# Kernel tuning notes

Hardware: AMD Instinct MI355X
Metric: run time of the kernel (lower is better)

Reference implementation:

```python
import jax, jax.numpy as jnp
import numpy as np

C_P = 1004.0
R_EARTH = 6371000.0
R_GAS = 287.0
OMEGA_E = 7.292e-05
B, K, H, W = 1, 8, 361, 720
KK = 5   # kernel basis size
D = 5    # neighborhood width in lat and lon (radius 2)
NS = K * 4 + 1
FCH = K * 4
NU = 2.0e5  # diffusion coefficient


def _ch(k, kind):
    return k * 4 + kind


def disco_gather(x, psi, quad):
    # DISCO sparse neighborhood aggregation on the sphere.
    # x: (B,C,H,W); psi: (KK,2,H,D,D) lat-dependent filter basis (2 directional comps)
    # returns (B,C,KK,2,H,W)
    Bx, C, Hx, Wx = x.shape
    Kk, nc, _, Dlat, Dlon = psi.shape
    r = Dlat // 2
    lat = np.clip(np.arange(Hx)[:, None] + np.arange(Dlat)[None, :] - r, 0, Hx - 1)
    out = jnp.zeros((Bx, C, Kk, nc, Hx, Wx), x.dtype)
    for dl in range(Dlat):
        li = lat[:, dl]
        xg = x[:, :, li, :] * quad[li][None, None, :, None]  # quadrature-weighted gather
        for dw in range(Dlon):
            xs = jnp.roll(xg, -(dw - r), axis=-1)  # circular in longitude
            out = out + psi[:, :, :, dl, dw][None, None, :, :, :, None] * xs[:, :, None, None, :, :]
    return out


def setup_inputs():
    key = jax.random.key(0)
    k1, k2, k3 = jax.random.split(key, 3)
    uv = jax.random.normal(k1, (B, K, H, W, 2), jnp.float32)
    T = jax.random.normal(k2, (B, K, H, W), jnp.float32)
    q = jax.random.normal(k3, (B, K, H, W), jnp.float32)
    rng = np.random.RandomState(0)
    psi = ((rng.rand(KK, 2, H, D, D) - 0.5) / (D * D)).astype(np.float32)
    colat = np.linspace(0.0, np.pi, H)
    quad = (np.sin(colat) * np.pi / (H - 1)).astype(np.float32)
    f_cor = (2.0 * OMEGA_E * np.sin(np.pi / 2.0 - colat)).astype(np.float32)
    p = np.array([1e5 * np.exp(-k * np.log(10.0) / (K - 1)) for k in range(K)], np.float32)
    lpr = np.log(p[:-1] / p[1:])
    p_low = np.concatenate([p[:1], 0.5 * (p[:-1] + p[1:])])
    p_up = np.concatenate([0.5 * (p[:-1] + p[1:]), [0.0]])
    dp = (p_low - p_up).astype(np.float32)
    # physics-encoded weights (module freezes all params and sets them analytically)
    W_ss_blk = np.zeros((NS, NS, KK), np.float32)
    W_vs_blk = np.zeros((NS, K, KK, 2), np.float32)
    for k in range(K):
        W_vs_blk[_ch(k, 2), k, :, 0] = 1.0 / R_EARTH  # zeta (curl)
        W_vs_blk[_ch(k, 3), k, :, 1] = 1.0 / R_EARTH  # div
    W_sv_blk = np.zeros((K, NS, KK, 2), np.float32)
    for ko in range(K):
        for ki in range(ko):
            W_sv_blk[ko, _ch(ki, 0), :, 1] = -R_GAS * lpr[ki] / R_EARTH  # PGF
        W_sv_blk[ko, _ch(ko, 1), :, 1] = -1.0 / R_EARTH  # -grad KE
    W_vv_blk = np.zeros((K, K, KK, 2), np.float32)
    W_vs2_blk = np.zeros((NS, K, KK, 2), np.float32)
    W_pw_ss = np.zeros((NS, NS), np.float32)
    W_pw_ss[FCH, FCH] = 1.0
    W_svp = np.zeros((NS, K, 2), np.float32)
    for k in range(K):
        W_svp[_ch(k, 2), k, 1] = 1.0
    W_svp[FCH, :, 1] = -1.0
    W_pw_vv = np.zeros((K, K), np.float32)
    W_ss_adv = np.zeros((2 * K, 2 * K, KK), np.float32)
    W_vs_adv = np.zeros((2 * K, K, KK, 2), np.float32)
    W_vs2_adv = np.zeros((2 * K, K, KK, 2), np.float32)
    for k in range(K):
        W_vs2_adv[k, k, :, 1] = -1.0 / R_EARTH      # -V.grad T
        W_vs2_adv[K + k, k, :, 1] = -1.0 / R_EARTH  # -V.grad q
    W_sv_grad = np.zeros((1, 1, KK, 2), np.float32)
    W_sv_grad[0, 0, :, 1] = 1.0 / R_EARTH
    W_vs_div = np.zeros((1, 1, KK, 2), np.float32)
    W_vs_div[0, 0, :, 1] = 1.0 / R_EARTH
    j = jnp.asarray
    return dict(uv=uv, T=T, q=q, psi=j(psi), quad=j(quad), f_cor=j(f_cor), p_levels=j(p), delta_p=j(dp),
                W_ss_blk=j(W_ss_blk), W_vs_blk=j(W_vs_blk), W_sv_blk=j(W_sv_blk), W_vv_blk=j(W_vv_blk),
                W_vs2_blk=j(W_vs2_blk), W_pw_ss=j(W_pw_ss), W_svp=j(W_svp), W_pw_vv=j(W_pw_vv),
                W_ss_adv=j(W_ss_adv), W_vs_adv=j(W_vs_adv), W_vs2_adv=j(W_vs2_adv),
                W_sv_grad=j(W_sv_grad), W_vs_div=j(W_vs_div))


def _forward(uv, T, q, psi, quad, f_cor, p_levels, delta_p, W_ss_blk, W_vs_blk, W_sv_blk, W_vv_blk,
             W_vs2_blk, W_pw_ss, W_svp, W_pw_vv, W_ss_adv, W_vs_adv, W_vs2_adv, W_sv_grad, W_vs_div):
    Bx, Kx, Hx, Wx = T.shape
    ke = 0.5 * (uv[..., 0] ** 2 + uv[..., 1] ** 2)
    zeros = jnp.zeros_like(T)
    per = jnp.stack([T, ke, zeros, zeros], axis=2).reshape(Bx, Kx * 4, Hx, Wx)
    f_field = jnp.broadcast_to(f_cor[None, None, :, None], (Bx, 1, Hx, Wx))
    x_s = jnp.concatenate([per, f_field], axis=1)  # (B, 4K+1, H, W)
    # ---- Block 1: VectorDiscoBlock ----
    Gs = disco_gather(x_s, psi, quad)               # (B,NS,KK,2,H,W)
    Ga = disco_gather(uv[..., 0], psi, quad)
    Gb = disco_gather(uv[..., 1], psi, quad)
    Gdir = jnp.stack([Ga[:, :, :, 0], Gb[:, :, :, 1]], axis=3)  # curl/div pairing
    Giso = jnp.stack([Ga[:, :, :, 0], Gb[:, :, :, 0]], axis=3)
    ys_c = jnp.einsum('oik,bikhw->bohw', W_ss_blk, Gs[:, :, :, 0])
    ys_c = ys_c + jnp.einsum('oikc,bikchw->bohw', W_vs_blk, Gdir)
    ys_c = ys_c + jnp.einsum('oikc,bokchw,bihwc->bohw', W_vs2_blk, Gs, uv)
    yv_c = jnp.einsum('oikc,bikchw->bohwc', W_sv_blk, Gs)
    yv_c = yv_c + jnp.einsum('oikc,bikchw->bohwc', W_vv_blk, Giso)
    s_feat = ys_c + jnp.einsum('oi,bihw->bohw', W_pw_ss, x_s)
    coef0 = jnp.einsum('ij,bihw->bjhw', W_svp[:, :, 0], s_feat)
    coef1 = jnp.einsum('ij,bihw->bjhw', W_svp[:, :, 1], s_feat)
    cross = jnp.stack([-uv[..., 1], uv[..., 0]], axis=-1)  # k-hat x V
    sv = coef0[..., None] * uv + coef1[..., None] * cross
    y_v = uv + yv_c + sv + jnp.einsum('oi,bihwc->bohwc', W_pw_vv, uv)
    y_s = s_feat
    duv_dt = y_v - uv
    # omega from divergence (upward pressure integral)
    div = y_s[:, :Kx * 4].reshape(Bx, Kx, 4, Hx, Wx)[:, :, 3]
    cum = jnp.cumsum(div * delta_p[None, :, None, None], axis=1)
    omega = 0.5 * (jnp.concatenate([jnp.zeros_like(cum[:, :1]), cum[:, :-1]], axis=1) + cum)
    # ---- adv_conv (W_vs2 pathway): -V.grad(T), -V.grad(q) ----
    tq = jnp.concatenate([T, q], axis=1)
    Gtq = disco_gather(tq, psi, quad)
    dTq = jnp.einsum('oik,bikhw->bohw', W_ss_adv, Gtq[:, :, :, 0])
    dTq = dTq + jnp.einsum('oikc,bikchw->bohw', W_vs_adv, Gdir)
    dTq = dTq + jnp.einsum('oikc,bokchw,bihwc->bohw', W_vs2_adv, Gtq, uv)
    dT_dt = dTq[:, :Kx]
    dq_dt = dTq[:, Kx:]
    # dT/dp central differences
    p = p_levels
    inter = (T[:, 2:] - T[:, :-2]) / (p[2:] - p[:-2])[None, :, None, None]
    first = (T[:, 1:2] - T[:, 0:1]) / (p[1] - p[0])
    last = (T[:, -1:] - T[:, -2:-1]) / (p[-1] - p[-2])
    dTdp = jnp.concatenate([first, inter, last], axis=1)
    pk = p[None, :, None, None]
    dT_dt = dT_dt + omega * (R_GAS / C_P * T / pk - dTdp)
    # ---- diffusion: nu * div(grad(s)) via grad_conv/div_conv ----
    def lap(s):
        sf = s.reshape(Bx * Kx, 1, Hx, Wx)
        Gsf = disco_gather(sf, psi, quad)
        g = jnp.einsum('oikc,bikchw->bohwc', W_sv_grad, Gsf)  # (BK,1,H,W,2)
        Gga = disco_gather(g[..., 0], psi, quad)
        Ggb = disco_gather(g[..., 1], psi, quad)
        Gd = jnp.stack([Gga[:, :, :, 0], Ggb[:, :, :, 1]], axis=3)
        return jnp.einsum('oikc,bikchw->bohw', W_vs_div, Gd).reshape(Bx, Kx, Hx, Wx)
    dT_dt = dT_dt + NU * lap(T)
    dq_dt = dq_dt + NU * lap(q)
    duv_dt = duv_dt + NU * jnp.stack([lap(uv[..., 0]), lap(uv[..., 1])], axis=-1)
    return duv_dt, dT_dt, dq_dt


def reference(uv, T, q, psi, quad, f_cor, p_levels, delta_p, W_ss_blk, W_vs_blk, W_sv_blk, W_vv_blk,
              W_vs2_blk, W_pw_ss, W_svp, W_pw_vv, W_ss_adv, W_vs_adv, W_vs2_adv, W_sv_grad, W_vs_div):
    return _forward(uv, T, q, psi, quad, f_cor, p_levels, delta_p, W_ss_blk, W_vs_blk, W_sv_blk,
                    W_vv_blk, W_vs2_blk, W_pw_ss, W_svp, W_pw_vv, W_ss_adv, W_vs_adv, W_vs2_adv,
                    W_sv_grad, W_vs_div)
```

## Files before the change

kernel.cpp:

```cpp
#include <hip/hip_runtime.h>


constexpr int Kz = 8, Hh = 361, Ww = 720;
constexpr int HW = Hh * Ww;
constexpr int OFF_DT = Kz * HW * 2;
constexpr int OFF_DQ = OFF_DT + Kz * HW;

constexpr int TH = 16, TW = 64;
constexpr int SH = TH + 8, SW4 = TW + 8;
constexpr int EH = TH + 4, EW4 = TW + 4;
constexpr int SW4P = 73;
constexpr int EW4P = 69;

__device__ __forceinline__ int clipH(int x) {
  return x < 0 ? 0 : (x > Hh - 1 ? Hh - 1 : x);
}

#define FMA4(acc, s, v)                                                        \
  do {                                                                         \
    acc.x = fmaf((s), (v).x, acc.x);                                           \
    acc.y = fmaf((s), (v).y, acc.y);                                           \
    acc.z = fmaf((s), (v).z, acc.z);                                           \
    acc.w = fmaf((s), (v).w, acc.w);                                           \
  } while (0)

#define ROWV(acc, a, b, c, d, e)                                               \
  do {                                                                         \
    FMA4(acc, wq0, a); FMA4(acc, wq1, b); FMA4(acc, wq2, c);                   \
    FMA4(acc, wq3, d); FMA4(acc, wq4, e);                                      \
  } while (0)

#define ROW5S(acc, q0, q1, q2, q3, q4, a, b, c, d, e)                          \
  acc = fmaf(q0, a, fmaf(q1, b, fmaf(q2, c, fmaf(q3, d, fmaf(q4, e, acc)))))

__global__ __launch_bounds__(256, 3) void pe_pass1(
    const float2* __restrict__ uv,
    const float*  __restrict__ Tg,
    const float*  __restrict__ qg,
    const float*  __restrict__ psi,
    const float*  __restrict__ quad,
    const float*  __restrict__ f_cor,
    const float*  __restrict__ delta_p,
    float* __restrict__ out,
    float2* __restrict__ ws)
{
  __shared__ float4 S4[SH][SW4P];
  __shared__ float4 d1S[EH][EW4P];
  __shared__ float P1q[EH][25];
  __shared__ float P0q[TH][25];

  const int tid = threadIdx.x;
  const int tx = tid & 15;
  const int ty = tid >> 4;
  const int w0 = blockIdx.x * TW;
  const int h0 = blockIdx.y * TH;
  const int k  = blockIdx.z;

  for (int idx = tid; idx < EH * 25; idx += 256) {
    int ee = idx / 25, t = idx - ee * 25;
    int p = clipH(h0 + ee - 2);
    int dl = t / 5;
    float s = 0.f;
    #pragma unroll
    for (int kk = 0; kk < 5; ++kk)
      s += psi[kk * (2 * Hh * 25) + Hh * 25 + p * 25 + t];
    P1q[ee][t] = s * quad[clipH(p + dl - 2)];
  }
  for (int idx = tid; idx < TH * 25; idx += 256) {
    int r = idx / 25, t = idx - r * 25;
    int p = clipH(h0 + r);
    int dl = t / 5;
    float s = 0.f;
    #pragma unroll
    for (int kk = 0; kk < 5; ++kk)
      s += psi[kk * (2 * Hh * 25) + p * 25 + t];
    P0q[r][t] = s * quad[clipH(p + dl - 2)];
  }

  for (int idx = tid; idx < SH * SW4; idx += 256) {
    int rr = idx / SW4, cc = idx - rr * SW4;
    int pr = clipH(h0 + rr - 4);
    int pc = w0 + cc - 4;
    pc = pc < 0 ? pc + Ww : (pc >= Ww ? pc - Ww : pc);
    int g = (k * Hh + pr) * Ww + pc;
    float2 uvv = uv[g];
    S4[rr][cc] = make_float4(uvv.x, uvv.y, Tg[g], qg[g]);
  }
  __syncthreads();

  for (int idx = tid; idx < EH * (EW4 / 4); idx += 256) {
    int ee = idx % EH;
    int gc = idx / EH;
    int cb = gc * 4;
    int p = clipH(h0 + ee - 2);
    float4 a0 = {0,0,0,0}, a1 = {0,0,0,0}, a2 = {0,0,0,0}, a3 = {0,0,0,0};
    #pragma unroll
    for (int dl = 0; dl < 5; ++dl) {
      int sp = clipH(p + dl - 2);
      int rr = sp - h0 + 4;
      const float4* row = &S4[rr][cb];
      float4 g0 = row[0], g1 = row[1], g2 = row[2], g3 = row[3];
      float4 g4 = row[4], g5 = row[5], g6 = row[6], g7 = row[7];
      const float* wr = &P1q[ee][dl * 5];
      float wq0 = wr[0], wq1 = wr[1], wq2 = wr[2], wq3 = wr[3], wq4 = wr[4];
      ROWV(a0, g0, g1, g2, g3, g4);
      ROWV(a1, g1, g2, g3, g4, g5);
      ROWV(a2, g2, g3, g4, g5, g6);
      ROWV(a3, g3, g4, g5, g6, g7);
    }
    d1S[ee][cb + 0] = a0; d1S[ee][cb + 1] = a1;
    d1S[ee][cb + 2] = a2; d1S[ee][cb + 3] = a3;
  }
  __syncthreads();

  const int h = h0 + ty;
  const int hc = h < Hh ? h : (Hh - 1);
  const int wbase = w0 + tx * 4;
  const float f = f_cor[hc];
  const float invR = (float)(1.0 / 6371000.0);
  const float halfInvR = 0.5f * invR;
  const float cL = 200000.0f * invR * invR;

  float4 lp0 = {0,0,0,0}, lp1 = {0,0,0,0}, lp2 = {0,0,0,0}, lp3 = {0,0,0,0};
  float du0 = 0.f, du1 = 0.f, du2 = 0.f, du3 = 0.f;
  float dk0 = 0.f, dk1 = 0.f, dk2 = 0.f, dk3 = 0.f;
  #pragma unroll
  for (int dl = 0; dl < 5; ++dl) {
    int sp = clipH(hc + dl - 2);
    int er = sp - h0 + 2;
    int rr = er + 2;
    const float* wr = &P1q[ty + 2][dl * 5];
    float wq0 = wr[0], wq1 = wr[1], wq2 = wr[2], wq3 = wr[3], wq4 = wr[4];
    {
      const float4* row = &d1S[er][tx * 4];
      float4 g0 = row[0], g1 = row[1], g2 = row[2], g3 = row[3];
      float4 g4 = row[4], g5 = row[5], g6 = row[6], g7 = row[7];
      ROWV(lp0, g0, g1, g2, g3, g4);
      ROWV(lp1, g1, g2, g3, g4, g5);
      ROWV(lp2, g2, g3, g4, g5, g6);
      ROWV(lp3, g3, g4, g5, g6, g7);
    }
    {
      const float4* srow = &S4[rr][tx * 4 + 2];
      float4 s0 = srow[0], s1 = srow[1], s2 = srow[2], s3 = srow[3];
      float4 s4 = srow[4], s5 = srow[5], s6 = srow[6], s7 = srow[7];
      float k0 = fmaf(s0.y, s0.y, s0.x * s0.x);
      float k1 = fmaf(s1.y, s1.y, s1.x * s1.x);
      float k2 = fmaf(s2.y, s2.y, s2.x * s2.x);
      float k3 = fmaf(s3.y, s3.y, s3.x * s3.x);
      float k4 = fmaf(s4.y, s4.y, s4.x * s4.x);
      float k5 = fmaf(s5.y, s5.y, s5.x * s5.x);
      float k6 = fmaf(s6.y, s6.y, s6.x * s6.x);
      float k7 = fmaf(s7.y, s7.y, s7.x * s7.x);
      ROW5S(dk0, wq0, wq1, wq2, wq3, wq4, k0, k1, k2, k3, k4);
      ROW5S(dk1, wq0, wq1, wq2, wq3, wq4, k1, k2, k3, k4, k5);
      ROW5S(dk2, wq0, wq1, wq2, wq3, wq4, k2, k3, k4, k5, k6);
      ROW5S(dk3, wq0, wq1, wq2, wq3, wq4, k3, k4, k5, k6, k7);
      const float* w0r = &P0q[ty][dl * 5];
      float q0 = w0r[0], q1 = w0r[1], q2 = w0r[2], q3 = w0r[3], q4 = w0r[4];
      ROW5S(du0, q0, q1, q2, q3, q4, s0.x, s1.x, s2.x, s3.x, s4.x);
      ROW5S(du1, q0, q1, q2, q3, q4, s1.x, s2.x, s3.x, s4.x, s5.x);
      ROW5S(du2, q0, q1, q2, q3, q4, s2.x, s3.x, s4.x, s5.x, s6.x);
      ROW5S(du3, q0, q1, q2, q3, q4, s3.x, s4.x, s5.x, s6.x, s7.x);
    }
  }

  if (h < Hh && wbase < Ww) {
    const float dpk = delta_p[k];
    float4 duvA, duvB, dTv, dqv, wsA, wsB;
    {
      float4 d1c = d1S[ty + 2][tx * 4 + 2];
      float4 ctr = S4[ty + 4][tx * 4 + 4];
      float coef1 = fmaf(du0, invR, -f);
      duvA.x = fmaf(-coef1, ctr.y, cL * lp0.x);
      duvA.y = fmaf(coef1, ctr.x, -halfInvR * dk0) + cL * lp0.y;
      dTv.x = -(invR * d1c.z) * ctr.y + cL * lp0.z;
      dqv.x = fmaf(-(invR * d1c.w), ctr.y, cL * lp0.w);
      wsA.x = invR * d1c.y * dpk; wsA.y = d1c.z;
    }
    {
      float4 d1c = d1S[ty + 2][tx * 4 + 3];
      float4 ctr = S4[ty + 4][tx * 4 + 5];
      float coef1 = fmaf(du1, invR, -f);
      duvA.z = fmaf(-coef1, ctr.y, cL * lp1.x);
      duvA.w = fmaf(coef1, ctr.x, -halfInvR * dk1) + cL * lp1.y;
      dTv.y = -(invR * d1c.z) * ctr.y + cL * lp1.z;
      dqv.y = fmaf(-(invR * d1c.w), ctr.y, cL * lp1.w);
      wsA.z = invR * d1c.y * dpk; wsA.w = d1c.z;
    }
    {
      float4 d1c = d1S[ty + 2][tx * 4 + 4];
      float4 ctr = S4[ty + 4][tx * 4 + 6];
      float coef1 = fmaf(du2, invR, -f);
      duvB.x = fmaf(-coef1, ctr.y, cL * lp2.x);
      duvB.y = fmaf(coef1, ctr.x, -halfInvR * dk2) + cL * lp2.y;
      dTv.z = -(invR * d1c.z) * ctr.y + cL * lp2.z;
      dqv.z = fmaf(-(invR * d1c.w), ctr.y, cL * lp2.w);
      wsB.x = invR * d1c.y * dpk; wsB.y = d1c.z;
    }
    {
      float4 d1c = d1S[ty + 2][tx * 4 + 5];
      float4 ctr = S4[ty + 4][tx * 4 + 7];
      float coef1 = fmaf(du3, invR, -f);
      duvB.z = fmaf(-coef1, ctr.y, cL * lp3.x);
      duvB.w = fmaf(coef1, ctr.x, -halfInvR * dk3) + cL * lp3.y;
      dTv.w = -(invR * d1c.z) * ctr.y + cL * lp3.z;
      dqv.w = fmaf(-(invR * d1c.w), ctr.y, cL * lp3.w);
      wsB.z = invR * d1c.y * dpk; wsB.w = d1c.z;
    }
    const int gidx = (k * Hh + h) * Ww + wbase;
    float4* o4 = (float4*)out;
    o4[gidx >> 1] = duvA;
    o4[(gidx >> 1) + 1] = duvB;
    *(float4*)&out[OFF_DT + gidx] = dTv;
    *(float4*)&out[OFF_DQ + gidx] = dqv;
    float4* w4 = (float4*)ws;
    w4[gidx >> 1] = wsA;
    w4[(gidx >> 1) + 1] = wsB;
  }
}

__global__ __launch_bounds__(256) void pe_pass2(
    const float* __restrict__ Tg,
    const float* __restrict__ p_levels,
    const float2* __restrict__ ws,
    float* __restrict__ out)
{
  int i2 = blockIdx.x * 256 + threadIdx.x;
  if (i2 >= HW / 2) return;
  const float invR = (float)(1.0 / 6371000.0);
  const float RCP = (float)(287.0 / 1004.0);

  float pl[Kz];
  #pragma unroll
  for (int k = 0; k < Kz; ++k) pl[k] = p_levels[k];

  const float2* T2 = (const float2*)Tg;
  const float4* ws4 = (const float4*)ws;
  float4* o4 = (float4*)out;
  float2* dT2 = (float2*)(out + OFF_DT);

  float2 cum = {0.f, 0.f}, sumT = {0.f, 0.f};
  float2 Tm = {0.f, 0.f}, Tc = T2[i2];

  #pragma unroll
  for (int k = 0; k < Kz; ++k) {
    float2 Tp = (k < Kz - 1) ? T2[(k + 1) * (HW / 2) + i2] : make_float2(0.f, 0.f);
    float4 wsv = ws4[k * (HW / 2) + i2];
    float om0 = fmaf(0.5f, wsv.x, cum.x); cum.x += wsv.x;
    float om1 = fmaf(0.5f, wsv.z, cum.y); cum.y += wsv.z;

    float dTdp0, dTdp1;
    if (k == 0) {
      float idp = 1.f / (pl[1] - pl[0]);
      dTdp0 = (Tp.x - Tc.x) * idp; dTdp1 = (Tp.y - Tc.y) * idp;
    } else if (k == Kz - 1) {
      float idp = 1.f / (pl[Kz - 1] - pl[Kz - 2]);
      dTdp0 = (Tc.x - Tm.x) * idp; dTdp1 = (Tc.y - Tm.y) * idp;
    } else {
      float idp = 1.f / (pl[k + 1] - pl[k - 1]);
      dTdp0 = (Tp.x - Tm.x) * idp; dTdp1 = (Tp.y - Tm.y) * idp;
    }
    float iplk = RCP / pl[k];
    float2 dt = dT2[k * (HW / 2) + i2];
    dt.x += om0 * (iplk * Tc.x - dTdp0);
    dt.y += om1 * (iplk * Tc.y - dTdp1);
    dT2[k * (HW / 2) + i2] = dt;

    float4 o = o4[k * (HW / 2) + i2];
    o.y += sumT.x; o.w += sumT.y;
    o4[k * (HW / 2) + i2] = o;

    if (k < Kz - 1) {
      float c = -287.0f * logf(pl[k] / pl[k + 1]) * invR;
      sumT.x = fmaf(c, wsv.y, sumT.x);
      sumT.y = fmaf(c, wsv.w, sumT.y);
    }
    Tm = Tc; Tc = Tp;
  }
}

constexpr int FTH = 16, FTW = 16;
constexpr int FSH = FTH + 8, FSW = FTW + 8;
constexpr int FEH = FTH + 4, FEW = FTW + 4;
constexpr int FSWp = FSW + 1, FEWp = FEW + 1;

__global__ __launch_bounds__(256) void pe_step(
    const float2* __restrict__ uv,
    const float*  __restrict__ Tg,
    const float*  __restrict__ qg,
    const float*  __restrict__ psi,
    const float*  __restrict__ quad,
    const float*  __restrict__ f_cor,
    const float*  __restrict__ p_levels,
    const float*  __restrict__ delta_p,
    float* __restrict__ out)
{
  __shared__ float uS[FSH][FSWp], vS[FSH][FSWp], TS[FSH][FSWp], qS[FSH][FSWp];
  __shared__ float keS[FEH][FEWp];
  __shared__ float d1uS[FEH][FEWp], d1vS[FEH][FEWp], d1TS[FEH][FEWp], d1qS[FEH][FEWp];
  __shared__ float P1L[FEH][25];
  __shared__ float P0L[FTH][25];
  __shared__ float quadA[FSH];
  __shared__ float pl[8], dps[8];

  const int tid = threadIdx.x;
  const int tx = tid & (FTW - 1);
  const int ty = tid >> 4;
  const int w0 = blockIdx.x * FTW;
  const int h0 = blockIdx.y * FTH;

  if (tid < FSH) quadA[tid] = quad[clipH(h0 + tid - 4)];
  if (tid < 8) { pl[tid] = p_levels[tid]; dps[tid] = delta_p[tid]; }
  for (int idx = tid; idx < FEH * 25; idx += 256) {
    int ee = idx / 25, t = idx - ee * 25;
    int p = clipH(h0 + ee - 2);
    float s = 0.f;
    #pragma unroll
    for (int kk = 0; kk < 5; ++kk)
      s += psi[kk * (2 * Hh * 25) + Hh * 25 + p * 25 + t];
    P1L[ee][t] = s;
  }
  for (int idx = tid; idx < FTH * 25; idx += 256) {
    int r = idx / 25, t = idx - r * 25;
    int p = clipH(h0 + r);
    float s = 0.f;
    #pragma unroll
    for (int kk = 0; kk < 5; ++kk)
      s += psi[kk * (2 * Hh * 25) + p * 25 + t];
    P0L[r][t] = s;
  }
  __syncthreads();

  const int h = h0 + ty;
  const bool act = h < Hh;
  const int hc = act ? h : (Hh - 1);
  const int w = w0 + tx;
  const float f = f_cor[hc];
  const float invR = (float)(1.0 / 6371000.0);
  const float cL = 200000.0f * invR * invR;
  const float RCP = (float)(287.0 / 1004.0);

  float cum = 0.f;
  float sumT = 0.f;

  #pragma unroll 1
  for (int k = 0; k < Kz; ++k) {
    __syncthreads();
    for (int idx = tid; idx < FSH * FSW; idx += 256) {
      int rr = idx / FSW, cc = idx - rr * FSW;
      int pr = clipH(h0 + rr - 4);
      int pc = w0 + cc - 4;
      pc = pc < 0 ? pc + Ww : (pc >= Ww ? pc - Ww : pc);
      int g = (k * Hh + pr) * Ww + pc;
      float2 uvv = uv[g];
      uS[rr][cc] = uvv.x; vS[rr][cc] = uvv.y;
      TS[rr][cc] = Tg[g]; qS[rr][cc] = qg[g];
    }
    __syncthreads();
    for (int idx = tid; idx < FEH * FEW; idx += 256) {
      int ee = idx / FEW, ec = idx - ee * FEW;
      float su = uS[ee + 2][ec + 2], sv = vS[ee + 2][ec + 2];
      keS[ee][ec] = 0.5f * (su * su + sv * sv);
    }
    for (int idx = tid; idx < FEH * FEW; idx += 256) {
      int ee = idx / FEW, ec = idx - ee * FEW;
      int p = clipH(h0 + ee - 2);
      float au = 0.f, av = 0.f, aT = 0.f, aq = 0.f;
      #pragma unroll
      for (int dl = 0; dl < 5; ++dl) {
        int sp = clipH(p + dl - 2);
        int rr = sp - h0 + 4;
        float qv = quadA[rr];
        float ru = 0.f, rv = 0.f, rT = 0.f, rq = 0.f;
        #pragma unroll
        for (int dw = 0; dw < 5; ++dw) {
          float wgt = P1L[ee][dl * 5 + dw];
          ru = fmaf(wgt, uS[rr][ec + dw], ru);
          rv = fmaf(wgt, vS[rr][ec + dw], rv);
          rT = fmaf(wgt, TS[rr][ec + dw], rT);
          rq = fmaf(wgt, qS[rr][ec + dw], rq);
        }
        au = fmaf(qv, ru, au); av = fmaf(qv, rv, av);
        aT = fmaf(qv, rT, aT); aq = fmaf(qv, rq, aq);
      }
      d1uS[ee][ec] = au; d1vS[ee][ec] = av;
      d1TS[ee][ec] = aT; d1qS[ee][ec] = aq;
    }
    __syncthreads();

    float d0u = 0.f, d1ke = 0.f;
    #pragma unroll
    for (int dl = 0; dl < 5; ++dl) {
      int sp = clipH(hc + dl - 2);
      int rr = sp - h0 + 4;
      int er = sp - h0 + 2;
      float qv = quadA[rr];
      float r0 = 0.f, rk = 0.f;
      #pragma unroll
      for (int dw = 0; dw < 5; ++dw) {
        r0 = fmaf(P0L[ty][dl * 5 + dw], uS[rr][tx + 2 + dw], r0);
        rk = fmaf(P1L[ty + 2][dl * 5 + dw], keS[er][tx + dw], rk);
      }
      d0u = fmaf(qv, r0, d0u);
      d1ke = fmaf(qv, rk, d1ke);
    }

    float lapu = 0.f, lapv = 0.f, lapT = 0.f, lapq = 0.f;
    #pragma unroll
    for (int dl = 0; dl < 5; ++dl) {
      int sp = clipH(hc + dl - 2);
      int er = sp - h0 + 2;
      float qv = quadA[er + 2];
      float ru = 0.f, rv = 0.f, rT = 0.f, rq = 0.f;
      #pragma unroll
      for (int dw = 0; dw < 5; ++dw) {
        float wgt = P1L[ty + 2][dl * 5 + dw];
        ru = fmaf(wgt, d1uS[er][tx + dw], ru);
        rv = fmaf(wgt, d1vS[er][tx + dw], rv);
        rT = fmaf(wgt, d1TS[er][tx + dw], rT);
        rq = fmaf(wgt, d1qS[er][tx + dw], rq);
      }
      lapu = fmaf(qv, ru, lapu); lapv = fmaf(qv, rv, lapv);
      lapT = fmaf(qv, rT, lapT); lapq = fmaf(qv, rq, lapq);
    }

    float d1T_c = d1TS[ty + 2][tx + 2];
    float d1v_c = d1vS[ty + 2][tx + 2];
    float d1q_c = d1qS[ty + 2][tx + 2];
    float uc = uS[ty + 4][tx + 4], vc = vS[ty + 4][tx + 4];
    float Tc = TS[ty + 4][tx + 4];

    float coef1 = fmaf(d0u, invR, -f);
    float duv0 = fmaf(-coef1, vc, cL * lapu);
    float yv1 = fmaf(-invR, d1ke, sumT);
    float duv1 = fmaf(coef1, uc, yv1) + cL * lapv;

    float div = invR * d1v_c;
    float dpk = dps[k];
    float omega = fmaf(0.5f * div, dpk, cum);
    cum = fmaf(div, dpk, cum);

    int gidx = (k * Hh + hc) * Ww + w;
    float dTdp;
    if (k == 0) {
      float Tp = Tg[gidx + HW];
      dTdp = (Tp - Tc) / (pl[1] - pl[0]);
    } else if (k == Kz - 1) {
      float Tm = Tg[gidx - HW];
      dTdp = (Tc - Tm) / (pl[Kz - 1] - pl[Kz - 2]);
    } else {
      float Tp = Tg[gidx + HW];
      float Tm = Tg[gidx - HW];
      dTdp = (Tp - Tm) / (pl[k + 1] - pl[k - 1]);
    }
    float adv = -(invR * d1T_c) * vc;
    float dT = adv + omega * ((RCP * Tc) / pl[k] - dTdp) + cL * lapT;
    float dq = fmaf(-(invR * d1q_c), vc, cL * lapq);

    if (act) {
      ((float2*)out)[(k * Hh + h) * Ww + w] = make_float2(duv0, duv1);
      out[OFF_DT + gidx] = dT;
      out[OFF_DQ + gidx] = dq;
    }

    if (k < Kz - 1) {
      float lpr = logf(pl[k] / pl[k + 1]);
      float wTk = (float)(-287.0 * (double)lpr / 6371000.0);
      sumT = fmaf(wTk, d1T_c, sumT);
    }
  }
}

extern "C" void kernel_launch(void* const* d_in, const int* in_sizes, int n_in,
                              void* d_out, int out_size, void* d_ws, size_t ws_size,
                              hipStream_t stream) {
  (void)in_sizes; (void)n_in; (void)out_size;
  const float2* uv   = (const float2*)d_in[0];
  const float*  T    = (const float*) d_in[1];
  const float*  q    = (const float*) d_in[2];
  const float*  psi  = (const float*) d_in[3];
  const float*  quad = (const float*) d_in[4];
  const float*  fc   = (const float*) d_in[5];
  const float*  pl   = (const float*) d_in[6];
  const float*  dp   = (const float*) d_in[7];

  const size_t ws_need = (size_t)Kz * HW * sizeof(float2);
  if (ws_size >= ws_need) {
    dim3 g1((Ww + TW - 1) / TW, (Hh + TH - 1) / TH, Kz);
    hipLaunchKernelGGL(pe_pass1, g1, dim3(256), 0, stream,
                       uv, T, q, psi, quad, fc, dp, (float*)d_out, (float2*)d_ws);
    dim3 g2((HW / 2 + 255) / 256);
    hipLaunchKernelGGL(pe_pass2, g2, dim3(256), 0, stream,
                       T, pl, (const float2*)d_ws, (float*)d_out);
  } else {
    dim3 grid(Ww / FTW, (Hh + FTH - 1) / FTH);
    hipLaunchKernelGGL(pe_step, grid, dim3(256), 0, stream,
                       uv, T, q, psi, quad, fc, pl, dp, (float*)d_out);
  }
}
```

Baseline: 79.43 us.

## Precompute psi-quad weight tables in separate kernel and widen pass2 vectorization

Adds a small pe_tables kernel that sums psi over the basis and multiplies by quadrature once per latitude. It writes padded rows (stride 40, float4-aligned) into workspace, and pass1 then reads weights straight from global/L2 instead of rebuilding per-block shared tables. This removes redundant per-block psi loads and a __syncthreads dependency, and frees shared memory. It adds one extra kernel launch and puts weight reads on the global load path. Pass2 now handles 4 columns per thread with float4 T/dT accesses to cut thread count and widen memory transactions.

```diff
diff --git a/kernel.cpp b/kernel.cpp
--- a/kernel.cpp
+++ b/kernel.cpp
@@ -11,6 +11,7 @@
 constexpr int EH = TH + 4, EW4 = TW + 4;
 constexpr int SW4P = 73;
 constexpr int EW4P = 69;
+constexpr int PROW = 40;
 
 __device__ __forceinline__ int clipH(int x) {
   return x < 0 ? 0 : (x > Hh - 1 ? Hh - 1 : x);
@@ -33,12 +34,33 @@
 #define ROW5S(acc, q0, q1, q2, q3, q4, a, b, c, d, e)                          \
   acc = fmaf(q0, a, fmaf(q1, b, fmaf(q2, c, fmaf(q3, d, fmaf(q4, e, acc)))))
 
+__global__ __launch_bounds__(256) void pe_tables(
+    const float* __restrict__ psi,
+    const float* __restrict__ quad,
+    float* __restrict__ P0g,
+    float* __restrict__ P1g)
+{
+  int idx = blockIdx.x * 256 + threadIdx.x;
+  if (idx >= Hh * 25) return;
+  int h = idx / 25, t = idx - h * 25;
+  int dl = t / 5, dw = t - dl * 5;
+  float s0 = 0.f, s1 = 0.f;
+  #pragma unroll
+  for (int kk = 0; kk < 5; ++kk) {
+    s0 += psi[kk * (2 * Hh * 25) + h * 25 + t];
+    s1 += psi[kk * (2 * Hh * 25) + Hh * 25 + h * 25 + t];
+  }
+  float qv = quad[clipH(h + dl - 2)];
+  P0g[h * PROW + dl * 8 + dw] = s0 * qv;
+  P1g[h * PROW + dl * 8 + dw] = s1 * qv;
+}
+
 __global__ __launch_bounds__(256, 3) void pe_pass1(
     const float2* __restrict__ uv,
     const float*  __restrict__ Tg,
     const float*  __restrict__ qg,
-    const float*  __restrict__ psi,
-    const float*  __restrict__ quad,
+    const float*  __restrict__ P0g,
+    const float*  __restrict__ P1g,
     const float*  __restrict__ f_cor,
     const float*  __restrict__ delta_p,
     float* __restrict__ out,
@@ -46,8 +68,6 @@
 {
   __shared__ float4 S4[SH][SW4P];
   __shared__ float4 d1S[EH][EW4P];
-  __shared__ float P1q[EH][25];
-  __shared__ float P0q[TH][25];
 
   const int tid = threadIdx.x;
   const int tx = tid & 15;
@@ -55,27 +75,6 @@
   const int w0 = blockIdx.x * TW;
   const int h0 = blockIdx.y * TH;
   const int k  = blockIdx.z;
-
-  for (int idx = tid; idx < EH * 25; idx += 256) {
-    int ee = idx / 25, t = idx - ee * 25;
-    int p = clipH(h0 + ee - 2);
-    int dl = t / 5;
-    float s = 0.f;
-    #pragma unroll
-    for (int kk = 0; kk < 5; ++kk)
-      s += psi[kk * (2 * Hh * 25) + Hh * 25 + p * 25 + t];
-    P1q[ee][t] = s * quad[clipH(p + dl - 2)];
-  }
-  for (int idx = tid; idx < TH * 25; idx += 256) {
-    int r = idx / 25, t = idx - r * 25;
-    int p = clipH(h0 + r);
-    int dl = t / 5;
-    float s = 0.f;
-    #pragma unroll
-    for (int kk = 0; kk < 5; ++kk)
-      s += psi[kk * (2 * Hh * 25) + p * 25 + t];
-    P0q[r][t] = s * quad[clipH(p + dl - 2)];
-  }
 
   for (int idx = tid; idx < SH * SW4; idx += 256) {
     int rr = idx / SW4, cc = idx - rr * SW4;
@@ -93,6 +92,7 @@
     int gc = idx / EH;
     int cb = gc * 4;
     int p = clipH(h0 + ee - 2);
+    const float* Pr = P1g + p * PROW;
     float4 a0 = {0,0,0,0}, a1 = {0,0,0,0}, a2 = {0,0,0,0}, a3 = {0,0,0,0};
     #pragma unroll
     for (int dl = 0; dl < 5; ++dl) {
@@ -101,8 +101,9 @@
       const float4* row = &S4[rr][cb];
       float4 g0 = row[0], g1 = row[1], g2 = row[2], g3 = row[3];
       float4 g4 = row[4], g5 = row[5], g6 = row[6], g7 = row[7];
-      const float* wr = &P1q[ee][dl * 5];
-      float wq0 = wr[0], wq1 = wr[1], wq2 = wr[2], wq3 = wr[3], wq4 = wr[4];
+      float4 wA = *(const float4*)(Pr + dl * 8);
+      float wq0 = wA.x, wq1 = wA.y, wq2 = wA.z, wq3 = wA.w;
+      float wq4 = Pr[dl * 8 + 4];
       ROWV(a0, g0, g1, g2, g3, g4);
       ROWV(a1, g1, g2, g3, g4, g5);
       ROWV(a2, g2, g3, g4, g5, g6);
@@ -120,6 +121,8 @@
   const float invR = (float)(1.0 / 6371000.0);
   const float halfInvR = 0.5f * invR;
   const float cL = 200000.0f * invR * invR;
+  const float* Pr1 = P1g + hc * PROW;
+  const float* Pr0 = P0g + hc * PROW;
 
   float4 lp0 = {0,0,0,0}, lp1 = {0,0,0,0}, lp2 = {0,0,0,0}, lp3 = {0,0,0,0};
   float du0 = 0.f, du1 = 0.f, du2 = 0.f, du3 = 0.f;
@@ -129,8 +132,9 @@
     int sp = clipH(hc + dl - 2);
     int er = sp - h0 + 2;
     int rr = er + 2;
-    const float* wr = &P1q[ty + 2][dl * 5];
-    float wq0 = wr[0], wq1 = wr[1], wq2 = wr[2], wq3 = wr[3], wq4 = wr[4];
+    float4 wA = *(const float4*)(Pr1 + dl * 8);
+    float wq0 = wA.x, wq1 = wA.y, wq2 = wA.z, wq3 = wA.w;
+    float wq4 = Pr1[dl * 8 + 4];
     {
       const float4* row = &d1S[er][tx * 4];
       float4 g0 = row[0], g1 = row[1], g2 = row[2], g3 = row[3];
@@ -156,8 +160,9 @@
       ROW5S(dk1, wq0, wq1, wq2, wq3, wq4, k1, k2, k3, k4, k5);
       ROW5S(dk2, wq0, wq1, wq2, wq3, wq4, k2, k3, k4, k5, k6);
       ROW5S(dk3, wq0, wq1, wq2, wq3, wq4, k3, k4, k5, k6, k7);
-      const float* w0r = &P0q[ty][dl * 5];
-      float q0 = w0r[0], q1 = w0r[1], q2 = w0r[2], q3 = w0r[3], q4 = w0r[4];
+      float4 w0A = *(const float4*)(Pr0 + dl * 8);
+      float q0 = w0A.x, q1 = w0A.y, q2 = w0A.z, q3 = w0A.w;
+      float q4 = Pr0[dl * 8 + 4];
       ROW5S(du0, q0, q1, q2, q3, q4, s0.x, s1.x, s2.x, s3.x, s4.x);
       ROW5S(du1, q0, q1, q2, q3, q4, s1.x, s2.x, s3.x, s4.x, s5.x);
       ROW5S(du2, q0, q1, q2, q3, q4, s2.x, s3.x, s4.x, s5.x, s6.x);
@@ -226,8 +231,8 @@
     const float2* __restrict__ ws,
     float* __restrict__ out)
 {
-  int i2 = blockIdx.x * 256 + threadIdx.x;
-  if (i2 >= HW / 2) return;
+  int i4 = blockIdx.x * 256 + threadIdx.x;
+  if (i4 >= HW / 4) return;
   const float invR = (float)(1.0 / 6371000.0);
   const float RCP = (float)(287.0 / 1004.0);
 
@@ -235,46 +240,59 @@
   #pragma unroll
   for (int k = 0; k < Kz; ++k) pl[k] = p_levels[k];
 
-  const float2* T2 = (const float2*)Tg;
+  const float4* T4 = (const float4*)Tg;
   const float4* ws4 = (const float4*)ws;
   float4* o4 = (float4*)out;
-  float2* dT2 = (float2*)(out + OFF_DT);
-
-  float2 cum = {0.f, 0.f}, sumT = {0.f, 0.f};
-  float2 Tm = {0.f, 0.f}, Tc = T2[i2];
+  float4* dT4 = (float4*)(out + OFF_DT);
+
+  float4 cum = {0,0,0,0}, sumT = {0,0,0,0};
+  float4 Tm = {0,0,0,0}, Tc = T4[i4];
 
   #pragma unroll
   for (int k = 0; k < Kz; ++k) {
-    float2 Tp = (k < Kz - 1) ? T2[(k + 1) * (HW / 2) + i2] : make_float2(0.f, 0.f);
-    float4 wsv = ws4[k * (HW / 2) + i2];
-    float om0 = fmaf(0.5f, wsv.x, cum.x); cum.x += wsv.x;
-    float om1 = fmaf(0.5f, wsv.z, cum.y); cum.y += wsv.z;
-
-    float dTdp0, dTdp1;
+    float4 Tp = (k < Kz - 1) ? T4[(k + 1) * (HW / 4) + i4] : make_float4(0,0,0,0);
+    float4 wa = ws4[k * (HW / 2) + 2 * i4];
+    float4 wb = ws4[k * (HW / 2) + 2 * i4 + 1];
+    float om0 = fmaf(0.5f, wa.x, cum.x); cum.x += wa.x;
+    float om1 = fmaf(0.5f, wa.z, cum.y); cum.y += wa.z;
+    float om2 = fmaf(0.5f, wb.x, cum.z); cum.z += wb.x;
+    float om3 = fmaf(0.5f, wb.z, cum.w); cum.w += wb.z;
+
+    float4 dTdp;
     if (k == 0) {
       float idp = 1.f / (pl[1] - pl[0]);
-      dTdp0 = (Tp.x - Tc.x) * idp; dTdp1 = (Tp.y - Tc.y) * idp;
+      dTdp.x = (Tp.x - Tc.x) * idp; dTdp.y = (Tp.y - Tc.y) * idp;
+      dTdp.z = (Tp.z - Tc.z) * idp; dTdp.w = (Tp.w - Tc.w) * idp;
     } else if (k == Kz - 1) {
       float idp = 1.f / (pl[Kz - 1] - pl[Kz - 2]);
-      dTdp0 = (Tc.x - Tm.x) * idp; dTdp1 = (Tc.y - Tm.y) * idp;
+      dTdp.x = (Tc.x - Tm.x) * idp; dTdp.y = (Tc.y - Tm.y) * idp;
+      dTdp.z = (Tc.z - Tm.z) * idp; dTdp.w = (Tc.w - Tm.w) * idp;
     } else {
       float idp = 1.f / (pl[k + 1] - pl[k - 1]);
-      dTdp0 = (Tp.x - Tm.x) * idp; dTdp1 = (Tp.y - Tm.y) * idp;
+      dTdp.x = (Tp.x - Tm.x) * idp; dTdp.y = (Tp.y - Tm.y) * idp;
+      dTdp.z = (Tp.z - Tm.z) * idp; dTdp.w = (Tp.w - Tm.w) * idp;
     }
     float iplk = RCP / pl[k];
-    float2 dt = dT2[k * (HW / 2) + i2];
-    dt.x += om0 * (iplk * Tc.x - dTdp0);
-    dt.y += om1 * (iplk * Tc.y - dTdp1);
-    dT2[k * (HW / 2) + i2] = dt;
-
-    float4 o = o4[k * (HW / 2) + i2];
-    o.y += sumT.x; o.w += sumT.y;
-    o4[k * (HW / 2) + i2] = o;
+    float4 dt = dT4[k * (HW / 4) + i4];
+    dt.x += om0 * fmaf(iplk, Tc.x, -dTdp.x);
+    dt.y += om1 * fmaf(iplk, Tc.y, -dTdp.y);
+    dt.z += om2 * fmaf(iplk, Tc.z, -dTdp.z);
+    dt.w += om3 * fmaf(iplk, Tc.w, -dTdp.w);
+    dT4[k * (HW / 4) + i4] = dt;
+
+    float4 oa = o4[k * (HW / 2) + 2 * i4];
+    float4 ob = o4[k * (HW / 2) + 2 * i4 + 1];
+    oa.y += sumT.x; oa.w += sumT.y;
+    ob.y += sumT.z; ob.w += sumT.w;
+    o4[k * (HW / 2) + 2 * i4] = oa;
+    o4[k * (HW / 2) + 2 * i4 + 1] = ob;
 
     if (k < Kz - 1) {
       float c = -287.0f * logf(pl[k] / pl[k + 1]) * invR;
-      sumT.x = fmaf(c, wsv.y, sumT.x);
-      sumT.y = fmaf(c, wsv.w, sumT.y);
+      sumT.x = fmaf(c, wa.y, sumT.x);
+      sumT.y = fmaf(c, wa.w, sumT.y);
+      sumT.z = fmaf(c, wb.y, sumT.z);
+      sumT.w = fmaf(c, wb.w, sumT.w);
     }
     Tm = Tc; Tc = Tp;
   }
@@ -485,12 +503,21 @@
   const float*  pl   = (const float*) d_in[6];
   const float*  dp   = (const float*) d_in[7];
 
-  const size_t ws_need = (size_t)Kz * HW * sizeof(float2);
+  const size_t ws_div_floats = (size_t)2 * Kz * HW;
+  const size_t ws_need = (ws_div_floats + 2 * Hh * PROW) * sizeof(float);
   if (ws_size >= ws_need) {
+    float* wsF = (float*)d_ws;
+    float* P0g = wsF + ws_div_floats;
+    float* P1g = P0g + Hh * PROW;
+
+    dim3 gt((Hh * 25 + 255) / 256);
+    hipLaunchKernelGGL(pe_tables, gt, dim3(256), 0, stream, psi, quad, P0g, P1g);
+
     dim3 g1((Ww + TW - 1) / TW, (Hh + TH - 1) / TH, Kz);
     hipLaunchKernelGGL(pe_pass1, g1, dim3(256), 0, stream,
-                       uv, T, q, psi, quad, fc, dp, (float*)d_out, (float2*)d_ws);
-    dim3 g2((HW / 2 + 255) / 256);
+                       uv, T, q, P0g, P1g, fc, dp, (float*)d_out, (float2*)d_ws);
+
+    dim3 g2((HW / 4 + 255) / 256);
     hipLaunchKernelGGL(pe_pass2, g2, dim3(256), 0, stream,
                        T, pl, (const float2*)d_ws, (float*)d_out);
   } else {
```

Measured after the change: 78.31 us. No clear change (-1.4%).
